# Optimization experiments

Measured on AMD Instinct MI355X. Metric: run time of the kernel, lower is better.

Reference implementation:

```python
import jax, jax.numpy as jnp
import numpy as np

RADIUS = 1.0
NSAMPLE = 32


def _query_ball(new_xyz, xyz, radius, nsample):
    # new_xyz (B,M,3), xyz (B,N,3) -> idx (B,M,nsample) int32
    B, M, _ = new_xyz.shape
    N = xyz.shape[1]
    # squared distances via ||q||^2 + ||p||^2 - 2 q.p (avoids BxMxNx3 diff tensor)
    q2 = jnp.sum(new_xyz * new_xyz, axis=-1)          # (B,M)
    p2 = jnp.sum(xyz * xyz, axis=-1)                  # (B,N)
    qp = jnp.einsum('bmd,bnd->bmn', new_xyz, xyz)     # (B,M,N)
    dist2 = q2[:, :, None] + p2[:, None, :] - 2.0 * qp
    mask = dist2 < radius * radius
    ar = jnp.arange(N, dtype=jnp.int32)
    masked = jnp.where(mask, ar[None, None, :], jnp.int32(N + 1))  # (B,M,N)
    first = jnp.sort(masked, axis=2)[:, :, :nsample]               # (B,M,S)
    first_valid = first[:, :, :1]                                   # pad with first neighbor
    idx = jnp.where(first == N + 1, first_valid, first)
    return idx.astype(jnp.int32)


def _group(points, idx):
    # points (B,C,N), idx (B,M,S) -> (B,C,M,S) gather along N
    B, C, N = points.shape
    M, S = idx.shape[1], idx.shape[2]
    ie = jnp.broadcast_to(idx.reshape(B, 1, M * S).astype(jnp.int32), (B, C, M * S))
    return jnp.take_along_axis(points, ie, axis=2).reshape(B, C, M, S)


def setup_inputs() -> dict:
    key = jax.random.key(0)
    k1, k2 = jax.random.split(key)
    B, N, M, C = 8, 8192, 2048, 64
    xyz = jax.random.normal(k1, (B, N, 3), dtype=jnp.float32)
    # centroids are a subset of the cloud -> every ball query has >= 1 valid neighbor
    new_xyz = xyz[:, :M, :]
    features = jax.random.normal(k2, (B, C, N), dtype=jnp.float32)
    return {"xyz": xyz, "new_xyz": new_xyz, "features": features}


def reference(xyz, new_xyz, features):
    idx = _query_ball(new_xyz, xyz, RADIUS, NSAMPLE)                      # (B,M,S)
    grouped_xyz = _group(jnp.swapaxes(xyz, 1, 2), idx)                    # (B,3,M,S)
    grouped_xyz = grouped_xyz - jnp.swapaxes(new_xyz, 1, 2)[..., None]    # recenter
    grouped_feat = _group(features, idx)                                  # (B,C,M,S)
    return jnp.concatenate([grouped_xyz, grouped_feat], axis=1)           # (B,3+C,M,S)
```

## Files before the change

### kernel.cpp

```cpp
#include <hip/hip_runtime.h>

#define N_PTS 8192
#define M_Q   2048
#define C_F   64
#define NS    32
#define B_SZ  8

__global__ __launch_bounds__(256) void qb_kernel(
    const float* __restrict__ xyz, const float* __restrict__ nxyz,
    int* __restrict__ idx_out)
{
#pragma clang fp contract(off)
    const int lane = threadIdx.x & 63;
    const int q    = blockIdx.x * 4 + (threadIdx.x >> 6);
    const int b    = q >> 11;
    const float* __restrict__ xb = xyz + (size_t)b * (N_PTS * 3);
    const float* __restrict__ qp = nxyz + (size_t)q * 3;
    const float qx = qp[0];
    const float qy = qp[1];
    const float qz = qp[2];
    const float q2 = (qx * qx + qy * qy) + qz * qz;
    int* __restrict__ out = idx_out + (size_t)q * NS;

    int  cnt = 0;
    int  first_idx = 0;
    bool have_first = false;

    for (int base = 0; base < N_PTS && cnt < NS; base += 256) {
        float d2[4];
#pragma unroll
        for (int cc = 0; cc < 4; ++cc) {
            const int n = base + cc * 64 + lane;
            const float* __restrict__ p = xb + n * 3;
            const float p0 = p[0], p1 = p[1], p2v = p[2];
            const float p2sum = (p0 * p0 + p1 * p1) + p2v * p2v;
            const float qpdot = (qx * p0 + qy * p1) + qz * p2v;
            d2[cc] = (q2 + p2sum) - 2.0f * qpdot;
        }
#pragma unroll
        for (int cc = 0; cc < 4; ++cc) {
            if (cnt >= NS) break;
            const bool pred = d2[cc] < 1.0f;
            const unsigned long long mask = __ballot(pred);
            if (mask) {
                if (!have_first) {
                    first_idx = base + cc * 64 + __ffsll(mask) - 1;
                    have_first = true;
                }
                if (pred) {
                    const int pos = cnt + (int)__popcll(mask & ((1ull << lane) - 1ull));
                    if (pos < NS) out[pos] = base + cc * 64 + lane;
                }
                cnt += (int)__popcll(mask);
            }
        }
    }
    if (cnt < NS) {
        for (int p = cnt + lane; p < NS; p += 64) out[p] = first_idx;
    }
}

__global__ __launch_bounds__(256) void transpose_kernel(
    const float* __restrict__ feat, float* __restrict__ featT)
{
    __shared__ float lds[C_F * 65];
    const int b  = blockIdx.x >> 7;
    const int n0 = (blockIdx.x & 127) * 64;

    {
        const int c4 = threadIdx.x >> 6;
        const int nn = threadIdx.x & 63;
#pragma unroll
        for (int k = 0; k < 16; ++k) {
            const int c = k * 4 + c4;
            lds[c * 65 + nn] = feat[((size_t)b * C_F + c) * N_PTS + n0 + nn];
        }
    }
    __syncthreads();
    {
        const int n4 = threadIdx.x >> 6;
        const int c  = threadIdx.x & 63;
#pragma unroll
        for (int k = 0; k < 16; ++k) {
            const int nn = k * 4 + n4;
            featT[((size_t)b * N_PTS + n0 + nn) * C_F + c] = lds[c * 65 + nn];
        }
    }
}

__global__ __launch_bounds__(256) void gather_kernel(
    const float* __restrict__ xyz, const float* __restrict__ nxyz,
    const float* __restrict__ featT, const int* __restrict__ idx,
    float* __restrict__ out)
{
    __shared__ float lds[67 * 33];
    const int q = blockIdx.x;
    const int b = q >> 11;
    const int m = q & (M_Q - 1);

    {
        const int p = threadIdx.x >> 3;
        const int j = threadIdx.x & 7;
        const int n = idx[q * NS + p];
        const float* __restrict__ fb = featT + ((size_t)b * N_PTS + n) * C_F;
#pragma unroll
        for (int k = 0; k < 2; ++k) {
            const int c = k * 32 + j * 4;
            const float4 v = *(const float4*)(fb + c);
            lds[(3 + c + 0) * 33 + p] = v.x;
            lds[(3 + c + 1) * 33 + p] = v.y;
            lds[(3 + c + 2) * 33 + p] = v.z;
            lds[(3 + c + 3) * 33 + p] = v.w;
        }
        if (j == 0) {
            const float* __restrict__ xb = xyz + (size_t)b * (N_PTS * 3) + (size_t)n * 3;
            const float* __restrict__ qp = nxyz + (size_t)q * 3;
            lds[0 * 33 + p] = xb[0] - qp[0];
            lds[1 * 33 + p] = xb[1] - qp[1];
            lds[2 * 33 + p] = xb[2] - qp[2];
        }
    }
    __syncthreads();

    {
        const size_t obase = ((size_t)b * 67 * M_Q + m) * NS;
#pragma unroll
        for (int it = 0; it < 9; ++it) {
            const int e = it * 256 + threadIdx.x;
            if (e < 67 * NS) {
                const int row = e >> 5;
                const int p   = e & 31;
                out[obase + (size_t)row * (M_Q * NS) + p] = lds[row * 33 + p];
            }
        }
    }
}

extern "C" void kernel_launch(void* const* d_in, const int* in_sizes, int n_in,
                              void* d_out, int out_size, void* d_ws, size_t ws_size,
                              hipStream_t stream)
{
    const float* xyz  = (const float*)d_in[0];
    const float* nxyz = (const float*)d_in[1];
    const float* feat = (const float*)d_in[2];
    float* out = (float*)d_out;

    int*   idx   = (int*)d_ws;
    float* featT = (float*)((char*)d_ws + (4 << 20));

    const int Q = B_SZ * M_Q;

    transpose_kernel<<<B_SZ * 128, 256, 0, stream>>>(feat, featT);
    qb_kernel<<<Q / 4, 256, 0, stream>>>(xyz, nxyz, idx);
    gather_kernel<<<Q, 256, 0, stream>>>(xyz, nxyz, featT, idx, out);
}
```

Measured before the change: 189.9 us.

## Fuse ball query with gather and precompute padded xyz with squared norms

Merges the ball-query and gather kernels into one kernel. Neighbor indices stay in shared memory instead of going through a global idx buffer, and each block processes four queries in sequence. A prep kernel now does the feature transpose and also packs xyz into float4 with the precomputed squared norm, so the query loop issues one vector load per point. Output stores are widened to float4. In exchange, the gather phase is serialized per block with extra barriers, and a block's gather cannot start until its slowest query wave finishes.

```diff
diff --git a/kernel.cpp b/kernel.cpp
--- a/kernel.cpp
+++ b/kernel.cpp
@@ -6,133 +6,142 @@
 #define NS    32
 #define B_SZ  8
 
-__global__ __launch_bounds__(256) void qb_kernel(
-    const float* __restrict__ xyz, const float* __restrict__ nxyz,
-    int* __restrict__ idx_out)
+__global__ __launch_bounds__(256) void prep_kernel(
+    const float* __restrict__ feat, const float* __restrict__ xyz,
+    float* __restrict__ featT, float4* __restrict__ xyz4)
 {
 #pragma clang fp contract(off)
-    const int lane = threadIdx.x & 63;
-    const int q    = blockIdx.x * 4 + (threadIdx.x >> 6);
-    const int b    = q >> 11;
-    const float* __restrict__ xb = xyz + (size_t)b * (N_PTS * 3);
-    const float* __restrict__ qp = nxyz + (size_t)q * 3;
-    const float qx = qp[0];
-    const float qy = qp[1];
-    const float qz = qp[2];
-    const float q2 = (qx * qx + qy * qy) + qz * qz;
-    int* __restrict__ out = idx_out + (size_t)q * NS;
-
-    int  cnt = 0;
-    int  first_idx = 0;
-    bool have_first = false;
-
-    for (int base = 0; base < N_PTS && cnt < NS; base += 256) {
-        float d2[4];
+    __shared__ float lds[C_F * 65];
+    if (blockIdx.x < B_SZ * 128) {
+        const int b  = blockIdx.x >> 7;
+        const int n0 = (blockIdx.x & 127) * 64;
+        {
+            const int c4 = threadIdx.x >> 6;
+            const int nn = threadIdx.x & 63;
 #pragma unroll
-        for (int cc = 0; cc < 4; ++cc) {
-            const int n = base + cc * 64 + lane;
-            const float* __restrict__ p = xb + n * 3;
-            const float p0 = p[0], p1 = p[1], p2v = p[2];
-            const float p2sum = (p0 * p0 + p1 * p1) + p2v * p2v;
-            const float qpdot = (qx * p0 + qy * p1) + qz * p2v;
-            d2[cc] = (q2 + p2sum) - 2.0f * qpdot;
-        }
-#pragma unroll
-        for (int cc = 0; cc < 4; ++cc) {
-            if (cnt >= NS) break;
-            const bool pred = d2[cc] < 1.0f;
-            const unsigned long long mask = __ballot(pred);
-            if (mask) {
-                if (!have_first) {
-                    first_idx = base + cc * 64 + __ffsll(mask) - 1;
-                    have_first = true;
-                }
-                if (pred) {
-                    const int pos = cnt + (int)__popcll(mask & ((1ull << lane) - 1ull));
-                    if (pos < NS) out[pos] = base + cc * 64 + lane;
-                }
-                cnt += (int)__popcll(mask);
+            for (int k = 0; k < 16; ++k) {
+                const int c = k * 4 + c4;
+                lds[c * 65 + nn] = feat[((size_t)b * C_F + c) * N_PTS + n0 + nn];
             }
         }
-    }
-    if (cnt < NS) {
-        for (int p = cnt + lane; p < NS; p += 64) out[p] = first_idx;
+        __syncthreads();
+        {
+            const int n4 = threadIdx.x >> 6;
+            const int c  = threadIdx.x & 63;
+#pragma unroll
+            for (int k = 0; k < 16; ++k) {
+                const int nn = k * 4 + n4;
+                featT[((size_t)b * N_PTS + n0 + nn) * C_F + c] = lds[c * 65 + nn];
+            }
+        }
+    } else {
+        const int i = (blockIdx.x - B_SZ * 128) * 256 + (int)threadIdx.x;
+        const float p0 = xyz[i * 3 + 0];
+        const float p1 = xyz[i * 3 + 1];
+        const float p2 = xyz[i * 3 + 2];
+        const float s  = (p0 * p0 + p1 * p1) + p2 * p2;
+        xyz4[i] = make_float4(p0, p1, p2, s);
     }
 }
 
-__global__ __launch_bounds__(256) void transpose_kernel(
-    const float* __restrict__ feat, float* __restrict__ featT)
+__global__ __launch_bounds__(256) void qbg_kernel(
+    const float4* __restrict__ xyz4, const float* __restrict__ nxyz,
+    const float* __restrict__ featT, float* __restrict__ out)
 {
-    __shared__ float lds[C_F * 65];
-    const int b  = blockIdx.x >> 7;
-    const int n0 = (blockIdx.x & 127) * 64;
+#pragma clang fp contract(off)
+    __shared__ int   sidx[4][NS];
+    __shared__ float stage[67 * 33];
+
+    const int lane = threadIdx.x & 63;
+    const int w    = threadIdx.x >> 6;
+    const int q    = blockIdx.x * 4 + w;
+    const int b    = q >> 11;
+    const float4* __restrict__ xb = xyz4 + (size_t)b * N_PTS;
 
     {
-        const int c4 = threadIdx.x >> 6;
-        const int nn = threadIdx.x & 63;
+        const float* __restrict__ qp = nxyz + (size_t)q * 3;
+        const float qx = qp[0], qy = qp[1], qz = qp[2];
+        const float q2 = (qx * qx + qy * qy) + qz * qz;
+
+        int  cnt = 0;
+        int  first_idx = 0;
+        bool have_first = false;
+
+        for (int base = 0; base < N_PTS && cnt < NS; base += 256) {
+            float4 P[4];
 #pragma unroll
-        for (int k = 0; k < 16; ++k) {
-            const int c = k * 4 + c4;
-            lds[c * 65 + nn] = feat[((size_t)b * C_F + c) * N_PTS + n0 + nn];
+            for (int cc = 0; cc < 4; ++cc)
+                P[cc] = xb[base + cc * 64 + lane];
+#pragma unroll
+            for (int cc = 0; cc < 4; ++cc) {
+                if (cnt >= NS) break;
+                const float qpdot = (qx * P[cc].x + qy * P[cc].y) + qz * P[cc].z;
+                const float d2 = (q2 + P[cc].w) - 2.0f * qpdot;
+                const bool pred = d2 < 1.0f;
+                const unsigned long long mask = __ballot(pred);
+                if (mask) {
+                    if (!have_first) {
+                        first_idx = base + cc * 64 + __ffsll(mask) - 1;
+                        have_first = true;
+                    }
+                    if (pred) {
+                        const int pos = cnt + (int)__popcll(mask & ((1ull << lane) - 1ull));
+                        if (pos < NS) sidx[w][pos] = base + cc * 64 + lane;
+                    }
+                    cnt += (int)__popcll(mask);
+                }
+            }
+        }
+        if (cnt < NS) {
+            for (int p = cnt + lane; p < NS; p += 64) sidx[w][p] = first_idx;
         }
     }
     __syncthreads();
-    {
-        const int n4 = threadIdx.x >> 6;
-        const int c  = threadIdx.x & 63;
-#pragma unroll
-        for (int k = 0; k < 16; ++k) {
-            const int nn = k * 4 + n4;
-            featT[((size_t)b * N_PTS + n0 + nn) * C_F + c] = lds[c * 65 + nn];
-        }
-    }
-}
 
-__global__ __launch_bounds__(256) void gather_kernel(
-    const float* __restrict__ xyz, const float* __restrict__ nxyz,
-    const float* __restrict__ featT, const int* __restrict__ idx,
-    float* __restrict__ out)
-{
-    __shared__ float lds[67 * 33];
-    const int q = blockIdx.x;
-    const int b = q >> 11;
-    const int m = q & (M_Q - 1);
+    const int pS = threadIdx.x >> 3;
+    const int j  = threadIdx.x & 7;
+    const size_t cstride = (size_t)M_Q * NS;
 
-    {
-        const int p = threadIdx.x >> 3;
-        const int j = threadIdx.x & 7;
-        const int n = idx[q * NS + p];
+    for (int w2 = 0; w2 < 4; ++w2) {
+        const int qq = blockIdx.x * 4 + w2;
+        const int mm = qq & (M_Q - 1);
+        const int n  = sidx[w2][pS];
+
         const float* __restrict__ fb = featT + ((size_t)b * N_PTS + n) * C_F;
 #pragma unroll
         for (int k = 0; k < 2; ++k) {
             const int c = k * 32 + j * 4;
             const float4 v = *(const float4*)(fb + c);
-            lds[(3 + c + 0) * 33 + p] = v.x;
-            lds[(3 + c + 1) * 33 + p] = v.y;
-            lds[(3 + c + 2) * 33 + p] = v.z;
-            lds[(3 + c + 3) * 33 + p] = v.w;
+            stage[(3 + c + 0) * 33 + pS] = v.x;
+            stage[(3 + c + 1) * 33 + pS] = v.y;
+            stage[(3 + c + 2) * 33 + pS] = v.z;
+            stage[(3 + c + 3) * 33 + pS] = v.w;
         }
         if (j == 0) {
-            const float* __restrict__ xb = xyz + (size_t)b * (N_PTS * 3) + (size_t)n * 3;
-            const float* __restrict__ qp = nxyz + (size_t)q * 3;
-            lds[0 * 33 + p] = xb[0] - qp[0];
-            lds[1 * 33 + p] = xb[1] - qp[1];
-            lds[2 * 33 + p] = xb[2] - qp[2];
+            const float4 pv = xb[n];
+            const float* __restrict__ qp2 = nxyz + (size_t)qq * 3;
+            stage[0 * 33 + pS] = pv.x - qp2[0];
+            stage[1 * 33 + pS] = pv.y - qp2[1];
+            stage[2 * 33 + pS] = pv.z - qp2[2];
         }
-    }
-    __syncthreads();
+        __syncthreads();
 
-    {
-        const size_t obase = ((size_t)b * 67 * M_Q + m) * NS;
+        const size_t obase = ((size_t)b * 67 * M_Q + mm) * NS;
 #pragma unroll
-        for (int it = 0; it < 9; ++it) {
-            const int e = it * 256 + threadIdx.x;
-            if (e < 67 * NS) {
-                const int row = e >> 5;
-                const int p   = e & 31;
-                out[obase + (size_t)row * (M_Q * NS) + p] = lds[row * 33 + p];
+        for (int it = 0; it < 3; ++it) {
+            const int e = it * 256 + (int)threadIdx.x;
+            if (e < 67 * 8) {
+                const int row  = e >> 3;
+                const int col4 = (e & 7) * 4;
+                float4 v;
+                v.x = stage[row * 33 + col4 + 0];
+                v.y = stage[row * 33 + col4 + 1];
+                v.z = stage[row * 33 + col4 + 2];
+                v.w = stage[row * 33 + col4 + 3];
+                *(float4*)&out[obase + (size_t)row * cstride + col4] = v;
             }
         }
+        __syncthreads();
     }
 }
 
@@ -145,12 +154,12 @@
     const float* feat = (const float*)d_in[2];
     float* out = (float*)d_out;
 
-    int*   idx   = (int*)d_ws;
-    float* featT = (float*)((char*)d_ws + (4 << 20));
+    float*  featT = (float*)d_ws;
+    float4* xyz4  = (float4*)((char*)d_ws + (20 << 20));
 
     const int Q = B_SZ * M_Q;
 
-    transpose_kernel<<<B_SZ * 128, 256, 0, stream>>>(feat, featT);
-    qb_kernel<<<Q / 4, 256, 0, stream>>>(xyz, nxyz, idx);
-    gather_kernel<<<Q, 256, 0, stream>>>(xyz, nxyz, featT, idx, out);
+    prep_kernel<<<B_SZ * 128 + (B_SZ * N_PTS) / 256, 256, 0, stream>>>(
+        feat, xyz, featT, xyz4);
+    qbg_kernel<<<Q / 4, 256, 0, stream>>>(xyz4, nxyz, featT, out);
 }
```

New measurement: 178.5 us. 6.0% less time.
